# Kernel optimization log

Measured on AMD Instinct MI355X. Metric: run time of the kernel, lower is better.

Reference implementation:

```python
import jax, jax.numpy as jnp
import numpy as np

B, N, E, D, H, M = 64, 4096, 8192, 256, 256, 64


def setup_inputs() -> dict:
    key = jax.random.key(0)
    ks = jax.random.split(key, 12)
    s = lambda fan_in: 1.0 / np.sqrt(fan_in)
    return {
        "node_embeddings": jax.random.normal(ks[0], (B, N, D), jnp.float32),
        "army_counts": jax.random.randint(ks[1], (B, N), 0, 50).astype(jnp.float32),
        "action_edges": jax.random.randint(ks[2], (B, E, 2), 0, N, dtype=jnp.int32),
        # edge_scorer: Linear(2H, H) -> ReLU -> Linear(H, 1)
        "W1": jax.random.normal(ks[3], (2 * H, H), jnp.float32) * s(2 * H),
        "b1": jnp.zeros((H,), jnp.float32),
        "W2": jax.random.normal(ks[4], (H, 1), jnp.float32) * s(H),
        "b2": jnp.zeros((1,), jnp.float32),
        # army_scorer: Linear(2D, 128) -> ReLU -> Linear(128, M)
        "A1": jax.random.normal(ks[5], (2 * D, 128), jnp.float32) * s(2 * D),
        "a1": jnp.zeros((128,), jnp.float32),
        "A2": jax.random.normal(ks[6], (128, M), jnp.float32) * s(128.0),
        "a2": jnp.zeros((M,), jnp.float32),
    }


def reference(node_embeddings, army_counts, W1, b1, W2, b2, A1, a1, A2, a2, action_edges):
    # node_embeddings: [B, N, D]; action_edges: [B, E, 2]; army_counts: [B, N]
    b, n, d = node_embeddings.shape
    m = A2.shape[1]
    dt = node_embeddings.dtype

    src = action_edges[..., 0]  # [B, E]
    tgt = action_edges[..., 1]
    src_c = jnp.clip(src, 0, n - 1)
    tgt_c = jnp.clip(tgt, 0, n - 1)

    # Gather endpoint embeddings: [B, E, D]
    src_e = jnp.take_along_axis(node_embeddings, src_c[..., None], axis=1)
    tgt_e = jnp.take_along_axis(node_embeddings, tgt_c[..., None], axis=1)
    edge_embed = jnp.concatenate([src_e, tgt_e], axis=-1)  # [B, E, 2D]

    # edge scorer MLP -> [B, E]
    h = jax.nn.relu(edge_embed @ W1 + b1)
    edge_logits = (h @ W2 + b2)[..., 0]

    # army scorer MLP -> [B, E, M]
    g = jax.nn.relu(edge_embed @ A1 + a1)
    army_logits = g @ A2 + a2

    src_armies = jnp.take_along_axis(army_counts, src_c, axis=1)  # [B, E]
    tgt_armies = jnp.take_along_axis(army_counts, tgt_c, axis=1)

    valid_edges = (src >= 0) & (tgt >= 0)
    bad_edges = valid_edges & ((src_armies <= 2) | (tgt_armies >= 3 * src_armies))
    edge_logits = edge_logits - bad_edges.astype(dt) * 1.0

    invalid_self = (src == tgt) & valid_edges
    edge_logits = edge_logits - invalid_self.astype(dt) * 100.0

    max_sendable = src_armies - 1  # [B, E]
    army_range = jnp.arange(m, dtype=dt)[None, None, :]  # [1, 1, M]
    valid_mask = army_range <= max_sendable[..., None]
    army_logits = jnp.where(valid_mask, army_logits, jnp.asarray(-1e9, dt))

    return edge_logits, army_logits
```

## Files before the change

kernel.cpp:

```cpp
#include <hip/hip_runtime.h>

#define BB   64
#define NN   4096
#define EE   8192
#define DD   256
#define HH   256
#define MM   64
#define K1   512
#define NC   384
#define TE   64
#define BLOCK 512
#define KC   32
#define NCHUNK 16
#define ASTR 40
#define GSTR 136
#define ABUF 2560
#define BE_TOT (BB * EE)
#define WCTF_ELEMS (NC * K1)
#define A2F_ELEMS  (128 * MM)
#define WS_NEEDED ((size_t)(WCTF_ELEMS + A2F_ELEMS) * sizeof(short))

typedef float f32x4 __attribute__((ext_vector_type(4)));
typedef short bf16x8 __attribute__((ext_vector_type(8)));

__device__ __forceinline__ short f2bf(float f) {
    unsigned u = __float_as_uint(f);
    unsigned r = (u + 0x7fffu + ((u >> 16) & 1u)) >> 16;
    return (short)r;
}

__device__ __forceinline__ void barrier_lgkm() {
    asm volatile("s_waitcnt lgkmcnt(0)\n\ts_barrier" ::: "memory");
}

__global__ void AttackHead_prep(const float* __restrict__ W1,
                                const float* __restrict__ A1,
                                const float* __restrict__ A2,
                                short* __restrict__ wctf,
                                short* __restrict__ a2f) {
    int t = blockIdx.x * 256 + threadIdx.x;
    if (t < 131072) {
        int k = t >> 8, n = t & 255;
        int c = k >> 5, kr = k & 31, quad = kr >> 3, j = kr & 7;
        int nt = n >> 4, l15 = n & 15;
        wctf[((c * 24 + nt) * 64 + quad * 16 + l15) * 8 + j] = f2bf(W1[t]);
    } else if (t < 131072 + 65536) {
        int t2 = t - 131072;
        int k = t2 >> 7, n = 256 + (t2 & 127);
        int c = k >> 5, kr = k & 31, quad = kr >> 3, j = kr & 7;
        int nt = n >> 4, l15 = n & 15;
        wctf[((c * 24 + nt) * 64 + quad * 16 + l15) * 8 + j] = f2bf(A1[t2]);
    } else if (t < 131072 + 65536 + 8192) {
        int t3 = t - 131072 - 65536;
        int k = t3 >> 6, n = t3 & 63;
        int ks = k >> 5, kr = k & 31, quad = kr >> 3, j = kr & 7;
        int nt2 = n >> 4, l15 = n & 15;
        a2f[((ks * 4 + nt2) * 64 + quad * 16 + l15) * 8 + j] = f2bf(A2[t3]);
    }
}

template <bool USE_WS>
__device__ __forceinline__ bf16x8 load_bfrag(const short* __restrict__ wf,
                                             const float* __restrict__ W1,
                                             const float* __restrict__ A1,
                                             int c, int nt, int lane) {
    if (USE_WS) {
        return *(const bf16x8*)(wf + ((c * 24 + nt) * 64 + lane) * 8);
    } else {
        int l15 = lane & 15, quad = lane >> 4;
        int n = nt * 16 + l15;
        bf16x8 r;
        #pragma unroll
        for (int j = 0; j < 8; ++j) {
            int k = c * KC + quad * 8 + j;
            float v = (n < HH) ? W1[k * HH + n] : A1[k * 128 + (n - HH)];
            r[j] = f2bf(v);
        }
        return r;
    }
}

template <bool USE_WS>
__device__ __forceinline__ bf16x8 load_a2frag(const short* __restrict__ a2f,
                                              const float* __restrict__ A2,
                                              int ks, int nt2, int lane) {
    if (USE_WS) {
        return *(const bf16x8*)(a2f + ((ks * 4 + nt2) * 64 + lane) * 8);
    } else {
        int l15 = lane & 15, quad = lane >> 4;
        int n = nt2 * 16 + l15;
        bf16x8 r;
        #pragma unroll
        for (int j = 0; j < 8; ++j) {
            int k = ks * 32 + quad * 8 + j;
            r[j] = f2bf(A2[k * MM + n]);
        }
        return r;
    }
}

template <bool USE_WS>
__global__ __launch_bounds__(BLOCK, 4)
void AttackHead_main(const float* __restrict__ nodes,
                     const float* __restrict__ army,
                     const int* __restrict__ edges,
                     const float* __restrict__ W1,
                     const float* __restrict__ b1,
                     const float* __restrict__ W2,
                     const float* __restrict__ b2,
                     const float* __restrict__ A1,
                     const float* __restrict__ a1,
                     const float* __restrict__ A2,
                     const float* __restrict__ a2,
                     const short* __restrict__ wctf,
                     const short* __restrict__ a2f,
                     float* __restrict__ out) {
    __shared__ __align__(16) short smem[8704];
    __shared__ int   srcn[TE], tgtn[TE];
    __shared__ float elog[TE], maxs[TE];

    const int tid = threadIdx.x;
    const int bb  = ((blockIdx.x & 7) << 10) | (blockIdx.x >> 3);
    const int bglob = bb >> 7;
    const long be0 = (long)bb * TE;

    if (tid < TE) {
        long be = be0 + tid;
        int src = edges[2 * be], tgt = edges[2 * be + 1];
        int sc = min(max(src, 0), NN - 1);
        int tc = min(max(tgt, 0), NN - 1);
        srcn[tid] = sc; tgtn[tid] = tc;
        float sa = army[(size_t)bglob * NN + sc];
        float ta = army[(size_t)bglob * NN + tc];
        bool valid = (src >= 0) && (tgt >= 0);
        bool bad   = valid && (sa <= 2.0f || ta >= 3.0f * sa);
        bool selfe = valid && (src == tgt);
        elog[tid] = b2[0] - (bad ? 1.0f : 0.0f) - (selfe ? 100.0f : 0.0f);
        maxs[tid] = sa - 1.0f;
    }

    const int w    = tid >> 6;
    const int lane = tid & 63;
    const int quad = lane >> 4;
    const int l15  = lane & 15;

    bf16x8 bfn0 = load_bfrag<USE_WS>(wctf, W1, A1, 0, w * 3 + 0, lane);
    bf16x8 bfn1 = load_bfrag<USE_WS>(wctf, W1, A1, 0, w * 3 + 1, lane);
    bf16x8 bfn2 = load_bfrag<USE_WS>(wctf, W1, A1, 0, w * 3 + 2, lane);

    __syncthreads();

    const int srow = tid >> 3;
    const int sj   = tid & 7;
    const size_t nbase_g = (size_t)bglob * NN;

    f32x4 acc[4][3] = {};

    {
        int node = srcn[srow];
        float4 v = *(const float4*)(nodes + (nbase_g + node) * DD + sj * 4);
        short4 s;
        s.x = f2bf(v.x); s.y = f2bf(v.y); s.z = f2bf(v.z); s.w = f2bf(v.w);
        *(short4*)(&smem[0 * ABUF + srow * ASTR + sj * 4]) = s;
    }
    float4 lda = *(const float4*)(nodes + (nbase_g + srcn[srow]) * DD + KC + sj * 4);

    int bufc = 0;
    for (int c = 0; c < NCHUNK; ++c) {
        barrier_lgkm();

        float4 ldn;
        if (c + 2 < NCHUNK) {
            int cc = c + 2;
            int node = (cc < 8) ? srcn[srow] : tgtn[srow];
            ldn = *(const float4*)(nodes + (nbase_g + node) * DD + (cc & 7) * KC + sj * 4);
        }

        bf16x8 bf0 = bfn0, bf1 = bfn1, bf2 = bfn2;
        if (c + 1 < NCHUNK) {
            bfn0 = load_bfrag<USE_WS>(wctf, W1, A1, c + 1, w * 3 + 0, lane);
            bfn1 = load_bfrag<USE_WS>(wctf, W1, A1, c + 1, w * 3 + 1, lane);
            bfn2 = load_bfrag<USE_WS>(wctf, W1, A1, c + 1, w * 3 + 2, lane);
        }

        const short* Ab = &smem[bufc * ABUF];
        bf16x8 af[4];
        #pragma unroll
        for (int mt = 0; mt < 4; ++mt)
            af[mt] = *(const bf16x8*)(&Ab[(mt * 16 + l15) * ASTR + quad * 8]);

        #pragma unroll
        for (int mt = 0; mt < 4; ++mt) {
            acc[mt][0] = __builtin_amdgcn_mfma_f32_16x16x32_bf16(af[mt], bf0, acc[mt][0], 0, 0, 0);
            acc[mt][1] = __builtin_amdgcn_mfma_f32_16x16x32_bf16(af[mt], bf1, acc[mt][1], 0, 0, 0);
            acc[mt][2] = __builtin_amdgcn_mfma_f32_16x16x32_bf16(af[mt], bf2, acc[mt][2], 0, 0, 0);
        }

        int bufw = (bufc + 1 == 3) ? 0 : bufc + 1;
        if (c + 1 < NCHUNK) {
            short4 s;
            s.x = f2bf(lda.x); s.y = f2bf(lda.y); s.z = f2bf(lda.z); s.w = f2bf(lda.w);
            *(short4*)(&smem[bufw * ABUF + srow * ASTR + sj * 4]) = s;
            lda = ldn;
        }
        bufc = bufw;
    }

    __syncthreads();

    short* Gs = smem;
    float ep[4][4] = {};
    #pragma unroll
    for (int jn = 0; jn < 3; ++jn) {
        int ct = (w * 3 + jn) * 16 + l15;
        float bias = (ct < HH) ? b1[ct] : a1[ct - HH];
        if (ct < HH) {
            float w2v = W2[ct];
            #pragma unroll
            for (int mt = 0; mt < 4; ++mt)
                #pragma unroll
                for (int r = 0; r < 4; ++r) {
                    float h = fmaxf(acc[mt][jn][r] + bias, 0.0f);
                    ep[mt][r] += h * w2v;
                }
        } else {
            int gc = ct - HH;
            #pragma unroll
            for (int mt = 0; mt < 4; ++mt)
                #pragma unroll
                for (int r = 0; r < 4; ++r) {
                    float g = fmaxf(acc[mt][jn][r] + bias, 0.0f);
                    Gs[(mt * 16 + quad * 4 + r) * GSTR + gc] = f2bf(g);
                }
        }
    }
    if (w < 6) {
        #pragma unroll
        for (int msk = 1; msk <= 8; msk <<= 1)
            #pragma unroll
            for (int mt = 0; mt < 4; ++mt)
                #pragma unroll
                for (int r = 0; r < 4; ++r)
                    ep[mt][r] += __shfl_xor(ep[mt][r], msk, 64);
        if (l15 == 0) {
            #pragma unroll
            for (int mt = 0; mt < 4; ++mt)
                #pragma unroll
                for (int r = 0; r < 4; ++r)
                    atomicAdd(&elog[mt * 16 + quad * 4 + r], ep[mt][r]);
        }
    }
    __syncthreads();

    const int mt2 = w >> 1;
    const int nh  = w & 1;
    f32x4 acc2[2] = {};
    #pragma unroll
    for (int ks = 0; ks < 4; ++ks) {
        bf16x8 ga = *(const bf16x8*)(&Gs[(mt2 * 16 + l15) * GSTR + ks * 32 + quad * 8]);
        #pragma unroll
        for (int nb = 0; nb < 2; ++nb) {
            bf16x8 bv = load_a2frag<USE_WS>(a2f, A2, ks, nh * 2 + nb, lane);
            acc2[nb] = __builtin_amdgcn_mfma_f32_16x16x32_bf16(ga, bv, acc2[nb], 0, 0, 0);
        }
    }

    if (tid < TE) out[be0 + tid] = elog[tid];

    #pragma unroll
    for (int nb = 0; nb < 2; ++nb) {
        int col = (nh * 2 + nb) * 16 + l15;
        float a2v = a2[col];
        #pragma unroll
        for (int r = 0; r < 4; ++r) {
            int grow = mt2 * 16 + quad * 4 + r;
            float val = acc2[nb][r] + a2v;
            if ((float)col > maxs[grow]) val = -1e9f;
            out[(size_t)BE_TOT + (size_t)(be0 + grow) * MM + col] = val;
        }
    }
}

extern "C" void kernel_launch(void* const* d_in, const int* in_sizes, int n_in,
                              void* d_out, int out_size, void* d_ws, size_t ws_size,
                              hipStream_t stream) {
    const float* nodes = (const float*)d_in[0];
    const float* army  = (const float*)d_in[1];
    const int*   edges = (const int*)d_in[2];
    const float* W1    = (const float*)d_in[3];
    const float* b1    = (const float*)d_in[4];
    const float* W2    = (const float*)d_in[5];
    const float* b2    = (const float*)d_in[6];
    const float* A1    = (const float*)d_in[7];
    const float* a1    = (const float*)d_in[8];
    const float* A2    = (const float*)d_in[9];
    const float* a2    = (const float*)d_in[10];
    float* out = (float*)d_out;

    int nblocks = BE_TOT / TE;

    if (ws_size >= WS_NEEDED) {
        short* wctf = (short*)d_ws;
        short* a2f  = wctf + WCTF_ELEMS;
        AttackHead_prep<<<800, 256, 0, stream>>>(W1, A1, A2, wctf, a2f);
        AttackHead_main<true><<<nblocks, BLOCK, 0, stream>>>(
            nodes, army, edges, W1, b1, W2, b2, A1, a1, A2, a2, wctf, a2f, out);
    } else {
        AttackHead_main<false><<<nblocks, BLOCK, 0, stream>>>(
            nodes, army, edges, W1, b1, W2, b2, A1, a1, A2, a2,
            (const short*)nullptr, (const short*)nullptr, out);
    }
}
```

Measured before the change: 661.4 us.

## Double K-chunk to 64, halve barriers, use packed bf16 conversion

Each staged A-tile chunk grows from 32 to 64 columns of K, so the main loop runs 8 iterations with 8 barriers instead of 16, and the LDS ring drops from three buffers to two. Weight fragments are loaded per 32-wide sub-step inside each iteration, and each thread now gathers two float4s per node row. The fp32-to-bf16 conversion switches from a software rounding routine to the hardware v_cvt_pk_bf16_f32 instruction, and the loop is fully unrolled. In exchange, each load is issued less far ahead, and register pressure rises at 4 waves per SIMD occupancy.

```diff
diff --git a/kernel.cpp b/kernel.cpp
--- a/kernel.cpp
+++ b/kernel.cpp
@@ -10,11 +10,12 @@
 #define NC   384
 #define TE   64
 #define BLOCK 512
-#define KC   32
-#define NCHUNK 16
-#define ASTR 40
+#define KC   64
+#define NCHUNK 8
+#define ASTR 88
 #define GSTR 136
-#define ABUF 2560
+#define ABUF (64 * ASTR)
+#define SMEM_SHORTS (2 * ABUF)
 #define BE_TOT (BB * EE)
 #define WCTF_ELEMS (NC * K1)
 #define A2F_ELEMS  (128 * MM)
@@ -27,6 +28,12 @@
     unsigned u = __float_as_uint(f);
     unsigned r = (u + 0x7fffu + ((u >> 16) & 1u)) >> 16;
     return (short)r;
+}
+
+__device__ __forceinline__ int cvt_pk_bf16(float lo, float hi) {
+    int r;
+    asm("v_cvt_pk_bf16_f32 %0, %1, %2" : "=v"(r) : "v"(lo), "v"(hi));
+    return r;
 }
 
 __device__ __forceinline__ void barrier_lgkm() {
@@ -72,7 +79,7 @@
         bf16x8 r;
         #pragma unroll
         for (int j = 0; j < 8; ++j) {
-            int k = c * KC + quad * 8 + j;
+            int k = c * 32 + quad * 8 + j;
             float v = (n < HH) ? W1[k * HH + n] : A1[k * 128 + (n - HH)];
             r[j] = f2bf(v);
         }
@@ -115,7 +122,7 @@
                      const short* __restrict__ wctf,
                      const short* __restrict__ a2f,
                      float* __restrict__ out) {
-    __shared__ __align__(16) short smem[8704];
+    __shared__ __align__(16) short smem[SMEM_SHORTS];
     __shared__ int   srcn[TE], tgtn[TE];
     __shared__ float elog[TE], maxs[TE];
 
@@ -144,66 +151,83 @@
     const int quad = lane >> 4;
     const int l15  = lane & 15;
 
-    bf16x8 bfn0 = load_bfrag<USE_WS>(wctf, W1, A1, 0, w * 3 + 0, lane);
-    bf16x8 bfn1 = load_bfrag<USE_WS>(wctf, W1, A1, 0, w * 3 + 1, lane);
-    bf16x8 bfn2 = load_bfrag<USE_WS>(wctf, W1, A1, 0, w * 3 + 2, lane);
+    bf16x8 bfc0 = load_bfrag<USE_WS>(wctf, W1, A1, 0, w * 3 + 0, lane);
+    bf16x8 bfc1 = load_bfrag<USE_WS>(wctf, W1, A1, 0, w * 3 + 1, lane);
+    bf16x8 bfc2 = load_bfrag<USE_WS>(wctf, W1, A1, 0, w * 3 + 2, lane);
 
     __syncthreads();
 
     const int srow = tid >> 3;
     const int sj   = tid & 7;
     const size_t nbase_g = (size_t)bglob * NN;
+    const float* srcp = nodes + (nbase_g + (size_t)srcn[srow]) * DD + sj * 8;
+    const float* tgtp = nodes + (nbase_g + (size_t)tgtn[srow]) * DD + sj * 8;
 
     f32x4 acc[4][3] = {};
 
     {
-        int node = srcn[srow];
-        float4 v = *(const float4*)(nodes + (nbase_g + node) * DD + sj * 4);
-        short4 s;
-        s.x = f2bf(v.x); s.y = f2bf(v.y); s.z = f2bf(v.z); s.w = f2bf(v.w);
-        *(short4*)(&smem[0 * ABUF + srow * ASTR + sj * 4]) = s;
-    }
-    float4 lda = *(const float4*)(nodes + (nbase_g + srcn[srow]) * DD + KC + sj * 4);
-
-    int bufc = 0;
+        float4 v0 = *(const float4*)(srcp);
+        float4 v1 = *(const float4*)(srcp + 4);
+        int4 s;
+        s.x = cvt_pk_bf16(v0.x, v0.y); s.y = cvt_pk_bf16(v0.z, v0.w);
+        s.z = cvt_pk_bf16(v1.x, v1.y); s.w = cvt_pk_bf16(v1.z, v1.w);
+        *(int4*)(&smem[srow * ASTR + sj * 8]) = s;
+    }
+    float4 lda0 = *(const float4*)(srcp + 64);
+    float4 lda1 = *(const float4*)(srcp + 68);
+
+    #pragma unroll
     for (int c = 0; c < NCHUNK; ++c) {
         barrier_lgkm();
 
-        float4 ldn;
+        float4 ldn0, ldn1;
         if (c + 2 < NCHUNK) {
-            int cc = c + 2;
-            int node = (cc < 8) ? srcn[srow] : tgtn[srow];
-            ldn = *(const float4*)(nodes + (nbase_g + node) * DD + (cc & 7) * KC + sj * 4);
-        }
-
-        bf16x8 bf0 = bfn0, bf1 = bfn1, bf2 = bfn2;
-        if (c + 1 < NCHUNK) {
-            bfn0 = load_bfrag<USE_WS>(wctf, W1, A1, c + 1, w * 3 + 0, lane);
-            bfn1 = load_bfrag<USE_WS>(wctf, W1, A1, c + 1, w * 3 + 1, lane);
-            bfn2 = load_bfrag<USE_WS>(wctf, W1, A1, c + 1, w * 3 + 2, lane);
-        }
-
-        const short* Ab = &smem[bufc * ABUF];
+            const float* p = ((c + 2) < 4 ? srcp : tgtp) + ((c + 2) & 3) * 64;
+            ldn0 = *(const float4*)(p);
+            ldn1 = *(const float4*)(p + 4);
+        }
+
+        bf16x8 bg0 = load_bfrag<USE_WS>(wctf, W1, A1, 2 * c + 1, w * 3 + 0, lane);
+        bf16x8 bg1 = load_bfrag<USE_WS>(wctf, W1, A1, 2 * c + 1, w * 3 + 1, lane);
+        bf16x8 bg2 = load_bfrag<USE_WS>(wctf, W1, A1, 2 * c + 1, w * 3 + 2, lane);
+
+        const short* Ab = &smem[(c & 1) * ABUF];
+
         bf16x8 af[4];
         #pragma unroll
         for (int mt = 0; mt < 4; ++mt)
             af[mt] = *(const bf16x8*)(&Ab[(mt * 16 + l15) * ASTR + quad * 8]);
-
         #pragma unroll
         for (int mt = 0; mt < 4; ++mt) {
-            acc[mt][0] = __builtin_amdgcn_mfma_f32_16x16x32_bf16(af[mt], bf0, acc[mt][0], 0, 0, 0);
-            acc[mt][1] = __builtin_amdgcn_mfma_f32_16x16x32_bf16(af[mt], bf1, acc[mt][1], 0, 0, 0);
-            acc[mt][2] = __builtin_amdgcn_mfma_f32_16x16x32_bf16(af[mt], bf2, acc[mt][2], 0, 0, 0);
-        }
-
-        int bufw = (bufc + 1 == 3) ? 0 : bufc + 1;
+            acc[mt][0] = __builtin_amdgcn_mfma_f32_16x16x32_bf16(af[mt], bfc0, acc[mt][0], 0, 0, 0);
+            acc[mt][1] = __builtin_amdgcn_mfma_f32_16x16x32_bf16(af[mt], bfc1, acc[mt][1], 0, 0, 0);
+            acc[mt][2] = __builtin_amdgcn_mfma_f32_16x16x32_bf16(af[mt], bfc2, acc[mt][2], 0, 0, 0);
+        }
+
         if (c + 1 < NCHUNK) {
-            short4 s;
-            s.x = f2bf(lda.x); s.y = f2bf(lda.y); s.z = f2bf(lda.z); s.w = f2bf(lda.w);
-            *(short4*)(&smem[bufw * ABUF + srow * ASTR + sj * 4]) = s;
-            lda = ldn;
-        }
-        bufc = bufw;
+            bfc0 = load_bfrag<USE_WS>(wctf, W1, A1, 2 * c + 2, w * 3 + 0, lane);
+            bfc1 = load_bfrag<USE_WS>(wctf, W1, A1, 2 * c + 2, w * 3 + 1, lane);
+            bfc2 = load_bfrag<USE_WS>(wctf, W1, A1, 2 * c + 2, w * 3 + 2, lane);
+        }
+
+        bf16x8 ag[4];
+        #pragma unroll
+        for (int mt = 0; mt < 4; ++mt)
+            ag[mt] = *(const bf16x8*)(&Ab[(mt * 16 + l15) * ASTR + 32 + quad * 8]);
+        #pragma unroll
+        for (int mt = 0; mt < 4; ++mt) {
+            acc[mt][0] = __builtin_amdgcn_mfma_f32_16x16x32_bf16(ag[mt], bg0, acc[mt][0], 0, 0, 0);
+            acc[mt][1] = __builtin_amdgcn_mfma_f32_16x16x32_bf16(ag[mt], bg1, acc[mt][1], 0, 0, 0);
+            acc[mt][2] = __builtin_amdgcn_mfma_f32_16x16x32_bf16(ag[mt], bg2, acc[mt][2], 0, 0, 0);
+        }
+
+        if (c + 1 < NCHUNK) {
+            int4 s;
+            s.x = cvt_pk_bf16(lda0.x, lda0.y); s.y = cvt_pk_bf16(lda0.z, lda0.w);
+            s.z = cvt_pk_bf16(lda1.x, lda1.y); s.w = cvt_pk_bf16(lda1.z, lda1.w);
+            *(int4*)(&smem[((c + 1) & 1) * ABUF + srow * ASTR + sj * 8]) = s;
+        }
+        if (c + 2 < NCHUNK) { lda0 = ldn0; lda1 = ldn1; }
     }
 
     __syncthreads();
```

Result: faster. 642.4 us (-2.9%).
